# Optimization experiments

Hardware: AMD Instinct MI355X
Metric: run time of the kernel (lower is better)

The kernel has to match this reference:

```python
import jax, jax.numpy as jnp
import numpy as np

B, S, D = 4, 2048, 512
H, DK, DV = 8, 64, 64


def setup_inputs() -> dict:
    key = jax.random.key(0)
    ks = jax.random.split(key, 12)
    inv = 1.0 / np.sqrt(D)
    return {
        "query": jax.random.normal(ks[0], (B, S, D), dtype=jnp.float32),
        "value": jax.random.normal(ks[1], (B, S, D), dtype=jnp.float32),
        "attention_mask": jax.random.randint(ks[2], (B, S), 0, 2, dtype=jnp.int32),
        "Wq": jax.random.normal(ks[3], (D, H * DK), dtype=jnp.float32) * inv,
        "bq": jnp.zeros((H * DK,), dtype=jnp.float32),
        "Wk": jax.random.normal(ks[4], (D, H * DK), dtype=jnp.float32) * inv,
        "bk": jnp.zeros((H * DK,), dtype=jnp.float32),
        "Wv": jax.random.normal(ks[5], (D, H * DV), dtype=jnp.float32) * inv,
        "bv": jnp.zeros((H * DV,), dtype=jnp.float32),
        "Wo": jax.random.normal(ks[6], (H * DV, D), dtype=jnp.float32) * inv,
        "bo": jnp.zeros((D,), dtype=jnp.float32),
    }


def _split_heads(x, h):
    b, s, _ = x.shape
    return x.reshape(b, s, h, -1).transpose(0, 2, 1, 3)  # (B,H,S,dh)


def reference(query, value, attention_mask, Wq, bq, Wk, bk, Wv, bv, Wo, bo):
    # QKV projections (activation=None -> identity); key defaults to value
    q = _split_heads(query @ Wq + bq, H)   # (B,H,S,DK)
    k = _split_heads(value @ Wk + bk, H)   # (B,H,S,DK)
    v = _split_heads(value @ Wv + bv, H)   # (B,H,S,DV)

    scores = jnp.einsum("bhqd,bhkd->bhqk", q, k) / jnp.sqrt(jnp.float32(DK))
    # additive mask: m = 1e9*(mask-1), applied on both key and query axes
    m = 1e9 * (attention_mask.astype(jnp.float32) - 1.0)  # (B,S)
    scores = scores + m[:, None, None, :] + m[:, None, :, None]

    weights = jax.nn.softmax(scores, axis=-1)
    ctx = jnp.einsum("bhqk,bhkd->bhqd", weights, v)        # (B,H,S,DV)
    ctx = ctx.transpose(0, 2, 1, 3).reshape(ctx.shape[0], ctx.shape[2], H * DV)
    return ctx @ Wo + bo  # (B,S,D)
```

## Files before the change

### kernel.cpp

```cpp
#include <hip/hip_runtime.h>

#define B_ 4
#define S_ 2048
#define D_ 512
#define H_ 8

typedef __attribute__((ext_vector_type(8))) __bf16 bf16x8;
typedef __attribute__((ext_vector_type(4))) float f32x4;

#define NEGBIG  -1.442695040e9f
#define QSCALE  0.18033688011112042f

__device__ __forceinline__ unsigned pack_rn(float a, float b) {
    union { float f; unsigned u; } ua, ub; ua.f = a; ub.f = b;
    return __builtin_amdgcn_perm(ub.u + 0x8000u, ua.u + 0x8000u, 0x07060302u);
}
__device__ __forceinline__ float b2f_lo(unsigned u) {
    union { unsigned u; float f; } v; v.u = u << 16; return v.f;
}
__device__ __forceinline__ float b2f_hi(unsigned u) {
    union { unsigned u; float f; } v; v.u = u & 0xFFFF0000u; return v.f;
}

__global__ __launch_bounds__(256) void cast_x(
    const float* __restrict__ q, const float* __restrict__ v,
    unsigned short* __restrict__ xq, unsigned short* __restrict__ xv)
{
    const float* src = blockIdx.z ? v : q;
    unsigned short* dst = blockIdx.z ? xv : xq;
    int i = (blockIdx.x * 256 + threadIdx.x) * 8;
    float4 f0 = *(const float4*)&src[i];
    float4 f1 = *(const float4*)&src[i + 4];
    uint4 o;
    o.x = pack_rn(f0.x, f0.y); o.y = pack_rn(f0.z, f0.w);
    o.z = pack_rn(f1.x, f1.y); o.w = pack_rn(f1.z, f1.w);
    *(uint4*)&dst[i] = o;
}

__global__ __launch_bounds__(256) void cast_wt(
    const float* __restrict__ Wq, const float* __restrict__ Wk,
    const float* __restrict__ Wv, const float* __restrict__ Wo,
    const int* __restrict__ amask,
    unsigned short* __restrict__ Tq, unsigned short* __restrict__ Tk,
    unsigned short* __restrict__ Tv, unsigned short* __restrict__ To,
    float* __restrict__ maskF)
{
    int z = blockIdx.z;
    int tid = threadIdx.x;
    if (z == 4) {
        int lin = (blockIdx.y * 8 + blockIdx.x) * 128 + tid;
        if (tid < 128) maskF[lin] = amask[lin] ? 0.f : NEGBIG;
        return;
    }
    const float* W = (z == 0) ? Wq : (z == 1) ? Wk : (z == 2) ? Wv : Wo;
    unsigned short* T = (z == 0) ? Tq : (z == 1) ? Tk : (z == 2) ? Tv : To;
    int n0 = blockIdx.x * 64, k0 = blockIdx.y * 64;

    __shared__ float Ts[64][69];
    #pragma unroll
    for (int it = 0; it < 4; it++) {
        int lin = tid + it * 256;
        int kr = lin >> 4, c4 = (lin & 15) * 4;
        float4 v = *(const float4*)&W[(k0 + kr) * 512 + n0 + c4];
        Ts[kr][c4 + 0] = v.x; Ts[kr][c4 + 1] = v.y;
        Ts[kr][c4 + 2] = v.z; Ts[kr][c4 + 3] = v.w;
    }
    __syncthreads();
    int n = tid >> 2, kc = tid & 3;
    unsigned p[8];
    #pragma unroll
    for (int j = 0; j < 8; j++)
        p[j] = pack_rn(Ts[kc * 16 + 2 * j][n], Ts[kc * 16 + 2 * j + 1][n]);
    unsigned short* dst = &T[(n0 + n) * 512 + k0 + kc * 16];
    *(uint4*)dst       = *(uint4*)&p[0];
    *(uint4*)(dst + 8) = *(uint4*)&p[4];
}

__global__ __launch_bounds__(256) void proj_qkv_mfma(
    const unsigned short* __restrict__ Xq, const unsigned short* __restrict__ Xv,
    const unsigned short* __restrict__ Wtq, const unsigned short* __restrict__ Wtk,
    const unsigned short* __restrict__ Wtv,
    const float* __restrict__ bq, const float* __restrict__ bk,
    const float* __restrict__ bv,
    unsigned short* __restrict__ Qb, unsigned short* __restrict__ Kb,
    unsigned short* __restrict__ VtG)
{
    const int z = blockIdx.z;
    const unsigned short* A  = (z == 0) ? Wtq : (z == 1) ? Wtk : Xv;
    const unsigned short* Bm = (z == 0) ? Xq  : (z == 1) ? Xv  : Wtv;
    const float* bias        = (z == 0) ? bq  : (z == 1) ? bk  : bv;
    const int m0 = (z < 2) ? blockIdx.y * 128 : blockIdx.x * 128;
    const int n0 = (z < 2) ? blockIdx.x * 128 : blockIdx.y * 128;

    const int tid = threadIdx.x;
    const int w = tid >> 6, lane = tid & 63;
    const int l15 = lane & 15, quad = lane >> 4;
    const int wm = (w >> 1) * 64, wn = (w & 1) * 64;

    __shared__ unsigned short As[128 * 72];
    __shared__ unsigned short Bs[128 * 72];

    f32x4 acc[4][4];
    #pragma unroll
    for (int i = 0; i < 4; i++)
        #pragma unroll
        for (int j = 0; j < 4; j++) acc[i][j] = (f32x4){0.f, 0.f, 0.f, 0.f};

    for (int k0 = 0; k0 < 512; k0 += 64) {
        __syncthreads();
        #pragma unroll
        for (int it = 0; it < 2; it++) {
            int lin = tid + it * 256;
            int row = lin >> 2, c2 = (lin & 3) * 2;
            *(uint4*)&As[row * 72 + c2 * 8]     = *(const uint4*)&A[(m0 + row) * 512 + k0 + c2 * 8];
            *(uint4*)&As[row * 72 + c2 * 8 + 8] = *(const uint4*)&A[(m0 + row) * 512 + k0 + c2 * 8 + 8];
            *(uint4*)&Bs[row * 72 + c2 * 8]     = *(const uint4*)&Bm[(n0 + row) * 512 + k0 + c2 * 8];
            *(uint4*)&Bs[row * 72 + c2 * 8 + 8] = *(const uint4*)&Bm[(n0 + row) * 512 + k0 + c2 * 8 + 8];
        }
        __syncthreads();
        #pragma unroll
        for (int kc = 0; kc < 2; kc++) {
            bf16x8 a[4], bb[4];
            #pragma unroll
            for (int i = 0; i < 4; i++)
                a[i] = *(const bf16x8*)&As[(wm + 16 * i + l15) * 72 + kc * 32 + quad * 8];
            #pragma unroll
            for (int j = 0; j < 4; j++)
                bb[j] = *(const bf16x8*)&Bs[(wn + 16 * j + l15) * 72 + kc * 32 + quad * 8];
            #pragma unroll
            for (int i = 0; i < 4; i++)
                #pragma unroll
                for (int j = 0; j < 4; j++)
                    acc[i][j] = __builtin_amdgcn_mfma_f32_16x16x32_bf16(a[i], bb[j], acc[i][j], 0, 0, 0);
        }
    }

    if (z == 2) {
        #pragma unroll
        for (int j = 0; j < 4; j++) {
            int N = n0 + wn + 16 * j + l15;
            float bv_ = bias[N];
            int h = N >> 6, d = N & 63;
            #pragma unroll
            for (int i = 0; i < 4; i++) {
                int Mb = m0 + wm + 16 * i + quad * 4;
                int b = Mb >> 11, s = Mb & 2047;
                uint2 o;
                o.x = pack_rn(acc[i][j][0] + bv_, acc[i][j][1] + bv_);
                o.y = pack_rn(acc[i][j][2] + bv_, acc[i][j][3] + bv_);
                *(uint2*)&VtG[((b * H_ + h) * 64 + d) * 2048 + s] = o;
            }
        }
    } else {
        unsigned short* dst = (z == 0) ? Qb : Kb;
        const float scale = (z == 0) ? QSCALE : 1.0f;
        #pragma unroll
        for (int j = 0; j < 4; j++) {
            int sg = n0 + wn + 16 * j + l15;
            int b = sg >> 11, s = sg & 2047;
            #pragma unroll
            for (int i = 0; i < 4; i++) {
                int F = m0 + wm + 16 * i + quad * 4;
                int h = F >> 6, d = F & 63;
                float4 b4 = *(const float4*)&bias[F];
                uint2 o;
                o.x = pack_rn((acc[i][j][0] + b4.x) * scale, (acc[i][j][1] + b4.y) * scale);
                o.y = pack_rn((acc[i][j][2] + b4.z) * scale, (acc[i][j][3] + b4.w) * scale);
                *(uint2*)&dst[((b * H_ + h) * 2048 + s) * 64 + d] = o;
            }
        }
    }
}

__global__ __launch_bounds__(256, 4) void flash_mfma(
    const unsigned short* __restrict__ Qg, const unsigned short* __restrict__ Kg,
    const unsigned short* __restrict__ VtG, const float* __restrict__ maskF,
    unsigned short* __restrict__ O0, unsigned short* __restrict__ O1,
    float* __restrict__ Lpart)
{
    const int bh = blockIdx.y, b = bh >> 3, h = bh & 7;
    const int q0 = blockIdx.x * 128;
    const int z  = blockIdx.z;
    const int kbeg = z * 1024;
    const int tid = threadIdx.x;
    const int w = tid >> 6, lane = tid & 63;
    const int l15 = lane & 15, quad = lane >> 4;

    __shared__ unsigned short Ks[2][64 * 72];
    __shared__ unsigned short Ps[4][32 * 72];
    __shared__ float Km[4][64];

    const float* mfb = maskF + b * 2048;
    unsigned short* pw = &Ps[w][0];

    bf16x8 qf[2][2];
    float mq[2];
    #pragma unroll
    for (int qb = 0; qb < 2; qb++) {
        int qrow = q0 + w * 32 + qb * 16 + l15;
        const unsigned short* p = &Qg[(bh * 2048 + qrow) * 64 + quad * 8];
        qf[qb][0] = *(const bf16x8*)p;
        qf[qb][1] = *(const bf16x8*)(p + 32);
        mq[qb] = mfb[qrow];
    }

    bf16x8 ones;
    #pragma unroll
    for (int i = 0; i < 8; i++) ones[i] = (__bf16)1.0f;

    const int srow = tid >> 2;
    const int sch  = (tid & 3) * 2;
    const unsigned short* kgb = Kg + (long)bh * 2048 * 64;

    *(uint4*)&Ks[0][srow * 72 + sch * 8]     = *(const uint4*)&kgb[(kbeg + srow) * 64 + sch * 8];
    *(uint4*)&Ks[0][srow * 72 + sch * 8 + 8] = *(const uint4*)&kgb[(kbeg + srow) * 64 + sch * 8 + 8];
    float mfreg = mfb[kbeg + lane];

    f32x4 accO[2][4];
    f32x4 accL[2];
    #pragma unroll
    for (int qb = 0; qb < 2; qb++) {
        accL[qb] = (f32x4){0.f, 0.f, 0.f, 0.f};
        #pragma unroll
        for (int dt = 0; dt < 4; dt++) accO[qb][dt] = (f32x4){0.f, 0.f, 0.f, 0.f};
    }

    __syncthreads();

    for (int tl = 0; tl < 16; tl++) {
        const int kt = kbeg + tl * 64;
        const int ktn = (tl < 15) ? kt + 64 : kt;
        const int cur = tl & 1, nxt = cur ^ 1;

        bf16x8 vf[4][2];
        #pragma unroll
        for (int dt = 0; dt < 4; dt++)
            #pragma unroll
            for (int kc = 0; kc < 2; kc++)
                vf[dt][kc] = *(const bf16x8*)&VtG[(bh * 64 + dt * 16 + l15) * 2048 + kt + kc * 32 + quad * 8];
        uint4 kst0 = *(const uint4*)&kgb[(ktn + srow) * 64 + sch * 8];
        uint4 kst1 = *(const uint4*)&kgb[(ktn + srow) * 64 + sch * 8 + 8];
        Km[w][lane] = mfreg;
        mfreg = mfb[ktn + lane];

        f32x4 kmf[4];
        #pragma unroll
        for (int nt = 0; nt < 4; nt++)
            kmf[nt] = *(const f32x4*)&Km[w][nt * 16 + quad * 4];

        bf16x8 kf[4][2];
        #pragma unroll
        for (int nt = 0; nt < 4; nt++)
            #pragma unroll
            for (int kc = 0; kc < 2; kc++)
                kf[nt][kc] = *(const bf16x8*)&Ks[cur][(nt * 16 + l15) * 72 + kc * 32 + quad * 8];
        f32x4 sc[2][4];
        #pragma unroll
        for (int qb = 0; qb < 2; qb++)
            #pragma unroll
            for (int nt = 0; nt < 4; nt++) {
                sc[qb][nt] = kmf[nt] + mq[qb];
                #pragma unroll
                for (int kc = 0; kc < 2; kc++)
                    sc[qb][nt] = __builtin_amdgcn_mfma_f32_16x16x32_bf16(
                        kf[nt][kc], qf[qb][kc], sc[qb][nt], 0, 0, 0);
            }

        #pragma unroll
        for (int qb = 0; qb < 2; qb++) {
            #pragma unroll
            for (int nt = 0; nt < 4; nt++) {
                float p0 = __builtin_amdgcn_exp2f(sc[qb][nt][0] - mq[qb]);
                float p1 = __builtin_amdgcn_exp2f(sc[qb][nt][1] - mq[qb]);
                float p2 = __builtin_amdgcn_exp2f(sc[qb][nt][2] - mq[qb]);
                float p3 = __builtin_amdgcn_exp2f(sc[qb][nt][3] - mq[qb]);
                uint2 pp;
                pp.x = pack_rn(p0, p1);
                pp.y = pack_rn(p2, p3);
                *(uint2*)&pw[(qb * 16 + l15) * 72 + nt * 16 + quad * 4] = pp;
            }
        }

        #pragma unroll
        for (int qb = 0; qb < 2; qb++) {
            bf16x8 pf0 = *(const bf16x8*)&pw[(qb * 16 + l15) * 72 + quad * 8];
            bf16x8 pf1 = *(const bf16x8*)&pw[(qb * 16 + l15) * 72 + 32 + quad * 8];
            accL[qb] = __builtin_amdgcn_mfma_f32_16x16x32_bf16(ones, pf0, accL[qb], 0, 0, 0);
            accL[qb] = __builtin_amdgcn_mfma_f32_16x16x32_bf16(ones, pf1, accL[qb], 0, 0, 0);
            #pragma unroll
            for (int dt = 0; dt < 4; dt++) {
                accO[qb][dt] = __builtin_amdgcn_mfma_f32_16x16x32_bf16(
                    vf[dt][0], pf0, accO[qb][dt], 0, 0, 0);
                accO[qb][dt] = __builtin_amdgcn_mfma_f32_16x16x32_bf16(
                    vf[dt][1], pf1, accO[qb][dt], 0, 0, 0);
            }
        }

        *(uint4*)&Ks[nxt][srow * 72 + sch * 8]     = kst0;
        *(uint4*)&Ks[nxt][srow * 72 + sch * 8 + 8] = kst1;
        __syncthreads();
    }

    unsigned short* Opz = z ? O1 : O0;
    float* Lz = Lpart + z * (32 * 2048);
    #pragma unroll
    for (int qb = 0; qb < 2; qb++) {
        int q = q0 + w * 32 + qb * 16 + l15;
        int obase = (b * 2048 + q) * 512 + h * 64 + quad * 4;
        #pragma unroll
        for (int dt = 0; dt < 4; dt++) {
            uint2 o;
            o.x = pack_rn(accO[qb][dt][0], accO[qb][dt][1]);
            o.y = pack_rn(accO[qb][dt][2], accO[qb][dt][3]);
            *(uint2*)&Opz[obase + dt * 16] = o;
        }
        if (quad == 0) Lz[bh * 2048 + q] = accL[qb][0];
    }
}

__global__ __launch_bounds__(256) void combine_ctx(
    const unsigned short* __restrict__ O0, const unsigned short* __restrict__ O1,
    const float* __restrict__ Lpart, unsigned short* __restrict__ ctx)
{
    int idx = blockIdx.x * 256 + threadIdx.x;
    int i4 = idx * 4;
    int bs = i4 >> 9;
    int h = (i4 & 511) >> 6;
    int b = bs >> 11, s = bs & 2047;
    int li_idx = ((b * 8 + h) << 11) + s;
    float inv = 1.f / (Lpart[li_idx] + Lpart[32 * 2048 + li_idx]);
    uint2 a = *(const uint2*)&O0[i4];
    uint2 c = *(const uint2*)&O1[i4];
    float o0 = (b2f_lo(a.x) + b2f_lo(c.x)) * inv;
    float o1 = (b2f_hi(a.x) + b2f_hi(c.x)) * inv;
    float o2 = (b2f_lo(a.y) + b2f_lo(c.y)) * inv;
    float o3 = (b2f_hi(a.y) + b2f_hi(c.y)) * inv;
    uint2 o;
    o.x = pack_rn(o0, o1);
    o.y = pack_rn(o2, o3);
    *(uint2*)&ctx[i4] = o;
}

__global__ __launch_bounds__(256) void proj_out_mfma(
    const unsigned short* __restrict__ ctxB, const unsigned short* __restrict__ Wto,
    const float* __restrict__ bo, float* __restrict__ out)
{
    const int m0 = blockIdx.y * 128, n0 = blockIdx.x * 128;
    const int tid = threadIdx.x;
    const int w = tid >> 6, lane = tid & 63;
    const int l15 = lane & 15, quad = lane >> 4;
    const int wm = (w >> 1) * 64, wn = (w & 1) * 64;

    __shared__ unsigned short As[128 * 72];
    __shared__ unsigned short Bs[128 * 72];

    f32x4 acc[4][4];
    #pragma unroll
    for (int i = 0; i < 4; i++)
        #pragma unroll
        for (int j = 0; j < 4; j++) acc[i][j] = (f32x4){0.f, 0.f, 0.f, 0.f};

    for (int k0 = 0; k0 < 512; k0 += 64) {
        __syncthreads();
        #pragma unroll
        for (int it = 0; it < 2; it++) {
            int lin = tid + it * 256;
            int row = lin >> 2, c2 = (lin & 3) * 2;
            *(uint4*)&As[row * 72 + c2 * 8]     = *(const uint4*)&Wto[(m0 + row) * 512 + k0 + c2 * 8];
            *(uint4*)&As[row * 72 + c2 * 8 + 8] = *(const uint4*)&Wto[(m0 + row) * 512 + k0 + c2 * 8 + 8];
            *(uint4*)&Bs[row * 72 + c2 * 8]     = *(const uint4*)&ctxB[(n0 + row) * 512 + k0 + c2 * 8];
            *(uint4*)&Bs[row * 72 + c2 * 8 + 8] = *(const uint4*)&ctxB[(n0 + row) * 512 + k0 + c2 * 8 + 8];
        }
        __syncthreads();
        #pragma unroll
        for (int kc = 0; kc < 2; kc++) {
            bf16x8 a[4], bb[4];
            #pragma unroll
            for (int i = 0; i < 4; i++)
                a[i] = *(const bf16x8*)&As[(wm + 16 * i + l15) * 72 + kc * 32 + quad * 8];
            #pragma unroll
            for (int j = 0; j < 4; j++)
                bb[j] = *(const bf16x8*)&Bs[(wn + 16 * j + l15) * 72 + kc * 32 + quad * 8];
            #pragma unroll
            for (int i = 0; i < 4; i++)
                #pragma unroll
                for (int j = 0; j < 4; j++)
                    acc[i][j] = __builtin_amdgcn_mfma_f32_16x16x32_bf16(a[i], bb[j], acc[i][j], 0, 0, 0);
        }
    }

    #pragma unroll
    for (int j = 0; j < 4; j++) {
        int sg = n0 + wn + 16 * j + l15;
        #pragma unroll
        for (int i = 0; i < 4; i++) {
            int F = m0 + wm + 16 * i + quad * 4;
            float4 b4 = *(const float4*)&bo[F];
            float4 vv;
            vv.x = acc[i][j][0] + b4.x;
            vv.y = acc[i][j][1] + b4.y;
            vv.z = acc[i][j][2] + b4.z;
            vv.w = acc[i][j][3] + b4.w;
            *(float4*)&out[sg * 512 + F] = vv;
        }
    }
}

extern "C" void kernel_launch(void* const* d_in, const int* in_sizes, int n_in,
                              void* d_out, int out_size, void* d_ws, size_t ws_size,
                              hipStream_t stream)
{
    const float* query = (const float*)d_in[0];
    const float* value = (const float*)d_in[1];
    const int*   amask = (const int*)d_in[2];
    const float* Wq = (const float*)d_in[3];
    const float* bq = (const float*)d_in[4];
    const float* Wk = (const float*)d_in[5];
    const float* bk = (const float*)d_in[6];
    const float* Wv = (const float*)d_in[7];
    const float* bv = (const float*)d_in[8];
    const float* Wo = (const float*)d_in[9];
    const float* bo = (const float*)d_in[10];
    float* out = (float*)d_out;

    char* ws = (char*)d_ws;
    const size_t MB = 1 << 20;
    unsigned short* Xbq = (unsigned short*)(ws);
    unsigned short* Xbv = (unsigned short*)(ws + 8 * MB);
    unsigned short* Wtq = (unsigned short*)(ws + 16 * MB);
    unsigned short* Wtk = (unsigned short*)(ws + 16 * MB + MB / 2);
    unsigned short* Wtv = (unsigned short*)(ws + 17 * MB);
    unsigned short* Wto = (unsigned short*)(ws + 17 * MB + MB / 2);
    unsigned short* Qb  = (unsigned short*)(ws + 18 * MB);
    unsigned short* Kb  = (unsigned short*)(ws + 26 * MB);
    unsigned short* VtG = (unsigned short*)(ws + 34 * MB);
    unsigned short* ctx = (unsigned short*)(ws + 42 * MB);
    float*          mF  = (float*)(ws + 50 * MB);
    float*          Lp  = (float*)(ws + 51 * MB);

    cast_x<<<dim3(2048, 1, 2), 256, 0, stream>>>(query, value, Xbq, Xbv);
    cast_wt<<<dim3(8, 8, 5), 256, 0, stream>>>(Wq, Wk, Wv, Wo, amask,
                                               Wtq, Wtk, Wtv, Wto, mF);
    proj_qkv_mfma<<<dim3(64, 4, 3), 256, 0, stream>>>(Xbq, Xbv, Wtq, Wtk, Wtv,
                                                      bq, bk, bv, Qb, Kb, VtG);
    flash_mfma<<<dim3(16, 32, 2), 256, 0, stream>>>(Qb, Kb, VtG, mF,
                                                    Xbq, Xbv, Lp);
    combine_ctx<<<dim3(4096), 256, 0, stream>>>(Xbq, Xbv, Lp, ctx);
    proj_out_mfma<<<dim3(64, 4), 256, 0, stream>>>(ctx, Wto, bo, out);
}
```

Measured before the change: 221.5 us.

## Fuse input cast and split-K combine into GEMMs, prefetch V, remap flash grid

Removes the separate fp32-to-bf16 cast kernel by converting query/value on the fly while loading tiles in the QKV projection. Removes the combine_ctx kernel by merging the two split-K partial outputs and normalising inside the output projection's B-tile load. Also double-buffers V fragments in registers in the flash kernel and remaps the flash grid to a 1D launch that groups blocks sharing the same head onto one XCD for L2 locality. This saves two launches and intermediate round-trips, at the cost of redundant per-tile conversion work and more register pressure in the flash kernel.

```diff
diff --git a/kernel.cpp b/kernel.cpp
--- a/kernel.cpp
+++ b/kernel.cpp
@@ -20,21 +20,6 @@
 }
 __device__ __forceinline__ float b2f_hi(unsigned u) {
     union { unsigned u; float f; } v; v.u = u & 0xFFFF0000u; return v.f;
-}
-
-__global__ __launch_bounds__(256) void cast_x(
-    const float* __restrict__ q, const float* __restrict__ v,
-    unsigned short* __restrict__ xq, unsigned short* __restrict__ xv)
-{
-    const float* src = blockIdx.z ? v : q;
-    unsigned short* dst = blockIdx.z ? xv : xq;
-    int i = (blockIdx.x * 256 + threadIdx.x) * 8;
-    float4 f0 = *(const float4*)&src[i];
-    float4 f1 = *(const float4*)&src[i + 4];
-    uint4 o;
-    o.x = pack_rn(f0.x, f0.y); o.y = pack_rn(f0.z, f0.w);
-    o.z = pack_rn(f1.x, f1.y); o.w = pack_rn(f1.z, f1.w);
-    *(uint4*)&dst[i] = o;
 }
 
 __global__ __launch_bounds__(256) void cast_wt(
@@ -77,7 +62,7 @@
 }
 
 __global__ __launch_bounds__(256) void proj_qkv_mfma(
-    const unsigned short* __restrict__ Xq, const unsigned short* __restrict__ Xv,
+    const float* __restrict__ Xq, const float* __restrict__ Xv,
     const unsigned short* __restrict__ Wtq, const unsigned short* __restrict__ Wtk,
     const unsigned short* __restrict__ Wtv,
     const float* __restrict__ bq, const float* __restrict__ bk,
@@ -86,8 +71,8 @@
     unsigned short* __restrict__ VtG)
 {
     const int z = blockIdx.z;
-    const unsigned short* A  = (z == 0) ? Wtq : (z == 1) ? Wtk : Xv;
-    const unsigned short* Bm = (z == 0) ? Xq  : (z == 1) ? Xv  : Wtv;
+    const float* Xf          = (z == 0) ? Xq : Xv;
+    const unsigned short* Wt = (z == 0) ? Wtq : (z == 1) ? Wtk : Wtv;
     const float* bias        = (z == 0) ? bq  : (z == 1) ? bk  : bv;
     const int m0 = (z < 2) ? blockIdx.y * 128 : blockIdx.x * 128;
     const int n0 = (z < 2) ? blockIdx.x * 128 : blockIdx.y * 128;
@@ -108,14 +93,28 @@
 
     for (int k0 = 0; k0 < 512; k0 += 64) {
         __syncthreads();
-        #pragma unroll
-        for (int it = 0; it < 2; it++) {
-            int lin = tid + it * 256;
-            int row = lin >> 2, c2 = (lin & 3) * 2;
-            *(uint4*)&As[row * 72 + c2 * 8]     = *(const uint4*)&A[(m0 + row) * 512 + k0 + c2 * 8];
-            *(uint4*)&As[row * 72 + c2 * 8 + 8] = *(const uint4*)&A[(m0 + row) * 512 + k0 + c2 * 8 + 8];
-            *(uint4*)&Bs[row * 72 + c2 * 8]     = *(const uint4*)&Bm[(n0 + row) * 512 + k0 + c2 * 8];
-            *(uint4*)&Bs[row * 72 + c2 * 8 + 8] = *(const uint4*)&Bm[(n0 + row) * 512 + k0 + c2 * 8 + 8];
+        {
+            unsigned short* Wdst = (z < 2) ? As : Bs;
+            const int wrow0 = (z < 2) ? m0 : n0;
+            #pragma unroll
+            for (int it = 0; it < 2; it++) {
+                int lin = tid + it * 256;
+                int row = lin >> 2, c2 = (lin & 3) * 2;
+                *(uint4*)&Wdst[row * 72 + c2 * 8]     = *(const uint4*)&Wt[(wrow0 + row) * 512 + k0 + c2 * 8];
+                *(uint4*)&Wdst[row * 72 + c2 * 8 + 8] = *(const uint4*)&Wt[(wrow0 + row) * 512 + k0 + c2 * 8 + 8];
+            }
+        }
+        {
+            unsigned short* Xdst = (z < 2) ? Bs : As;
+            const int xrow0 = (z < 2) ? n0 : m0;
+            #pragma unroll
+            for (int it = 0; it < 8; it++) {
+                int lin = tid + it * 256;
+                int row = lin >> 4, c4 = (lin & 15) * 4;
+                float4 v = *(const float4*)&Xf[(xrow0 + row) * 512 + k0 + c4];
+                uint2 pp; pp.x = pack_rn(v.x, v.y); pp.y = pack_rn(v.z, v.w);
+                *(uint2*)&Xdst[row * 72 + c4] = pp;
+            }
         }
         __syncthreads();
         #pragma unroll
@@ -178,9 +177,13 @@
     unsigned short* __restrict__ O0, unsigned short* __restrict__ O1,
     float* __restrict__ Lpart)
 {
-    const int bh = blockIdx.y, b = bh >> 3, h = bh & 7;
-    const int q0 = blockIdx.x * 128;
-    const int z  = blockIdx.z;
+    const int lin = blockIdx.x;
+    const int xcd = lin & 7, slot = lin >> 3;
+    const int qi = slot & 15, pp = slot >> 4;
+    const int pair = xcd * 8 + pp;
+    const int bh = pair >> 1, z = pair & 1;
+    const int b = bh >> 3, h = bh & 7;
+    const int q0 = qi * 128;
     const int kbeg = z * 1024;
     const int tid = threadIdx.x;
     const int w = tid >> 6, lane = tid & 63;
@@ -211,10 +214,18 @@
     const int srow = tid >> 2;
     const int sch  = (tid & 3) * 2;
     const unsigned short* kgb = Kg + (long)bh * 2048 * 64;
+    const unsigned short* vgb = VtG + (long)bh * 64 * 2048;
 
     *(uint4*)&Ks[0][srow * 72 + sch * 8]     = *(const uint4*)&kgb[(kbeg + srow) * 64 + sch * 8];
     *(uint4*)&Ks[0][srow * 72 + sch * 8 + 8] = *(const uint4*)&kgb[(kbeg + srow) * 64 + sch * 8 + 8];
     float mfreg = mfb[kbeg + lane];
+
+    bf16x8 vf[2][4][2];
+    #pragma unroll
+    for (int dt = 0; dt < 4; dt++)
+        #pragma unroll
+        for (int kc = 0; kc < 2; kc++)
+            vf[0][dt][kc] = *(const bf16x8*)&vgb[(dt * 16 + l15) * 2048 + kbeg + kc * 32 + quad * 8];
 
     f32x4 accO[2][4];
     f32x4 accL[2];
@@ -232,12 +243,11 @@
         const int ktn = (tl < 15) ? kt + 64 : kt;
         const int cur = tl & 1, nxt = cur ^ 1;
 
-        bf16x8 vf[4][2];
         #pragma unroll
         for (int dt = 0; dt < 4; dt++)
             #pragma unroll
             for (int kc = 0; kc < 2; kc++)
-                vf[dt][kc] = *(const bf16x8*)&VtG[(bh * 64 + dt * 16 + l15) * 2048 + kt + kc * 32 + quad * 8];
+                vf[nxt][dt][kc] = *(const bf16x8*)&vgb[(dt * 16 + l15) * 2048 + ktn + kc * 32 + quad * 8];
         uint4 kst0 = *(const uint4*)&kgb[(ktn + srow) * 64 + sch * 8];
         uint4 kst1 = *(const uint4*)&kgb[(ktn + srow) * 64 + sch * 8 + 8];
         Km[w][lane] = mfreg;
@@ -274,10 +284,10 @@
                 float p1 = __builtin_amdgcn_exp2f(sc[qb][nt][1] - mq[qb]);
                 float p2 = __builtin_amdgcn_exp2f(sc[qb][nt][2] - mq[qb]);
                 float p3 = __builtin_amdgcn_exp2f(sc[qb][nt][3] - mq[qb]);
-                uint2 pp;
-                pp.x = pack_rn(p0, p1);
-                pp.y = pack_rn(p2, p3);
-                *(uint2*)&pw[(qb * 16 + l15) * 72 + nt * 16 + quad * 4] = pp;
+                uint2 pp2;
+                pp2.x = pack_rn(p0, p1);
+                pp2.y = pack_rn(p2, p3);
+                *(uint2*)&pw[(qb * 16 + l15) * 72 + nt * 16 + quad * 4] = pp2;
             }
         }
 
@@ -290,9 +300,9 @@
             #pragma unroll
             for (int dt = 0; dt < 4; dt++) {
                 accO[qb][dt] = __builtin_amdgcn_mfma_f32_16x16x32_bf16(
-                    vf[dt][0], pf0, accO[qb][dt], 0, 0, 0);
+                    vf[cur][dt][0], pf0, accO[qb][dt], 0, 0, 0);
                 accO[qb][dt] = __builtin_amdgcn_mfma_f32_16x16x32_bf16(
-                    vf[dt][1], pf1, accO[qb][dt], 0, 0, 0);
+                    vf[cur][dt][1], pf1, accO[qb][dt], 0, 0, 0);
             }
         }
 
@@ -318,31 +328,9 @@
     }
 }
 
-__global__ __launch_bounds__(256) void combine_ctx(
+__global__ __launch_bounds__(256) void proj_out_mfma(
     const unsigned short* __restrict__ O0, const unsigned short* __restrict__ O1,
-    const float* __restrict__ Lpart, unsigned short* __restrict__ ctx)
-{
-    int idx = blockIdx.x * 256 + threadIdx.x;
-    int i4 = idx * 4;
-    int bs = i4 >> 9;
-    int h = (i4 & 511) >> 6;
-    int b = bs >> 11, s = bs & 2047;
-    int li_idx = ((b * 8 + h) << 11) + s;
-    float inv = 1.f / (Lpart[li_idx] + Lpart[32 * 2048 + li_idx]);
-    uint2 a = *(const uint2*)&O0[i4];
-    uint2 c = *(const uint2*)&O1[i4];
-    float o0 = (b2f_lo(a.x) + b2f_lo(c.x)) * inv;
-    float o1 = (b2f_hi(a.x) + b2f_hi(c.x)) * inv;
-    float o2 = (b2f_lo(a.y) + b2f_lo(c.y)) * inv;
-    float o3 = (b2f_hi(a.y) + b2f_hi(c.y)) * inv;
-    uint2 o;
-    o.x = pack_rn(o0, o1);
-    o.y = pack_rn(o2, o3);
-    *(uint2*)&ctx[i4] = o;
-}
-
-__global__ __launch_bounds__(256) void proj_out_mfma(
-    const unsigned short* __restrict__ ctxB, const unsigned short* __restrict__ Wto,
+    const float* __restrict__ Lpart, const unsigned short* __restrict__ Wto,
     const float* __restrict__ bo, float* __restrict__ out)
 {
     const int m0 = blockIdx.y * 128, n0 = blockIdx.x * 128;
@@ -361,6 +349,7 @@
         for (int j = 0; j < 4; j++) acc[i][j] = (f32x4){0.f, 0.f, 0.f, 0.f};
 
     for (int k0 = 0; k0 < 512; k0 += 64) {
+        const int h = k0 >> 6;
         __syncthreads();
         #pragma unroll
         for (int it = 0; it < 2; it++) {
@@ -368,8 +357,26 @@
             int row = lin >> 2, c2 = (lin & 3) * 2;
             *(uint4*)&As[row * 72 + c2 * 8]     = *(const uint4*)&Wto[(m0 + row) * 512 + k0 + c2 * 8];
             *(uint4*)&As[row * 72 + c2 * 8 + 8] = *(const uint4*)&Wto[(m0 + row) * 512 + k0 + c2 * 8 + 8];
-            *(uint4*)&Bs[row * 72 + c2 * 8]     = *(const uint4*)&ctxB[(n0 + row) * 512 + k0 + c2 * 8];
-            *(uint4*)&Bs[row * 72 + c2 * 8 + 8] = *(const uint4*)&ctxB[(n0 + row) * 512 + k0 + c2 * 8 + 8];
+            int srow = n0 + row;
+            int b = srow >> 11, s = srow & 2047;
+            int li_idx = ((b * 8 + h) << 11) + s;
+            float inv = 1.f / (Lpart[li_idx] + Lpart[32 * 2048 + li_idx]);
+            long gofs = (long)srow * 512 + k0 + c2 * 8;
+            #pragma unroll
+            for (int half = 0; half < 2; half++) {
+                uint4 a4 = *(const uint4*)&O0[gofs + half * 8];
+                uint4 c4 = *(const uint4*)&O1[gofs + half * 8];
+                uint4 o4;
+                o4.x = pack_rn((b2f_lo(a4.x) + b2f_lo(c4.x)) * inv,
+                               (b2f_hi(a4.x) + b2f_hi(c4.x)) * inv);
+                o4.y = pack_rn((b2f_lo(a4.y) + b2f_lo(c4.y)) * inv,
+                               (b2f_hi(a4.y) + b2f_hi(c4.y)) * inv);
+                o4.z = pack_rn((b2f_lo(a4.z) + b2f_lo(c4.z)) * inv,
+                               (b2f_hi(a4.z) + b2f_hi(c4.z)) * inv);
+                o4.w = pack_rn((b2f_lo(a4.w) + b2f_lo(c4.w)) * inv,
+                               (b2f_hi(a4.w) + b2f_hi(c4.w)) * inv);
+                *(uint4*)&Bs[row * 72 + c2 * 8 + half * 8] = o4;
+            }
         }
         __syncthreads();
         #pragma unroll
@@ -425,8 +432,8 @@
 
     char* ws = (char*)d_ws;
     const size_t MB = 1 << 20;
-    unsigned short* Xbq = (unsigned short*)(ws);
-    unsigned short* Xbv = (unsigned short*)(ws + 8 * MB);
+    unsigned short* O0  = (unsigned short*)(ws);
+    unsigned short* O1  = (unsigned short*)(ws + 8 * MB);
     unsigned short* Wtq = (unsigned short*)(ws + 16 * MB);
     unsigned short* Wtk = (unsigned short*)(ws + 16 * MB + MB / 2);
     unsigned short* Wtv = (unsigned short*)(ws + 17 * MB);
@@ -434,17 +441,13 @@
     unsigned short* Qb  = (unsigned short*)(ws + 18 * MB);
     unsigned short* Kb  = (unsigned short*)(ws + 26 * MB);
     unsigned short* VtG = (unsigned short*)(ws + 34 * MB);
-    unsigned short* ctx = (unsigned short*)(ws + 42 * MB);
     float*          mF  = (float*)(ws + 50 * MB);
     float*          Lp  = (float*)(ws + 51 * MB);
 
-    cast_x<<<dim3(2048, 1, 2), 256, 0, stream>>>(query, value, Xbq, Xbv);
     cast_wt<<<dim3(8, 8, 5), 256, 0, stream>>>(Wq, Wk, Wv, Wo, amask,
                                                Wtq, Wtk, Wtv, Wto, mF);
-    proj_qkv_mfma<<<dim3(64, 4, 3), 256, 0, stream>>>(Xbq, Xbv, Wtq, Wtk, Wtv,
+    proj_qkv_mfma<<<dim3(64, 4, 3), 256, 0, stream>>>(query, value, Wtq, Wtk, Wtv,
                                                       bq, bk, bv, Qb, Kb, VtG);
-    flash_mfma<<<dim3(16, 32, 2), 256, 0, stream>>>(Qb, Kb, VtG, mF,
-                                                    Xbq, Xbv, Lp);
-    combine_ctx<<<dim3(4096), 256, 0, stream>>>(Xbq, Xbv, Lp, ctx);
-    proj_out_mfma<<<dim3(64, 4), 256, 0, stream>>>(ctx, Wto, bo, out);
-}
+    flash_mfma<<<dim3(1024), 256, 0, stream>>>(Qb, Kb, VtG, mF, O0, O1, Lp);
+    proj_out_mfma<<<dim3(64, 4), 256, 0, stream>>>(O0, O1, Lp, Wto, bo, out);
+}
```

Measured after the change: 344.5 us. +55.5%, slower.
